# Kernel optimization log

Measured on AMD Instinct MI355X. Metric: run time of the kernel, lower is better.

Reference implementation:

```python
import jax, jax.numpy as jnp
from jax import lax
import numpy as np

B, T_IN, NF, H, T_OUT = 2048, 336, 16, 128, 168


def _gru_cell(x, h, Wih, Whh, bih, bhh):
    # PyTorch GRU cell, gate order [r, z, n]
    gi = x @ Wih.T + bih          # (B, 3H)
    gh = h @ Whh.T + bhh          # (B, 3H)
    i_r, i_z, i_n = jnp.split(gi, 3, axis=-1)
    h_r, h_z, h_n = jnp.split(gh, 3, axis=-1)
    r = jax.nn.sigmoid(i_r + h_r)
    z = jax.nn.sigmoid(i_z + h_z)
    n = jnp.tanh(i_n + r * h_n)
    return (1.0 - z) * n + z * h


def _run_gru_layer(seq_tbf, Wih, Whh, bih, bhh):
    # seq_tbf: (T, B, in_dim) -> (outputs (T,B,H), final hidden (B,H))
    h0 = jnp.zeros((seq_tbf.shape[1], H), seq_tbf.dtype)
    def step(h, xt):
        h2 = _gru_cell(xt, h, Wih, Whh, bih, bhh)
        return h2, h2
    hT, ys = lax.scan(step, h0, seq_tbf)
    return ys, hT


def setup_inputs() -> dict:
    key = jax.random.key(0)
    ks = iter(jax.random.split(key, 32))
    def w(shape, fan):
        return (jax.random.normal(next(ks), shape, jnp.float32) / np.sqrt(fan).astype(np.float32))
    inp = {"x": jax.random.normal(next(ks), (B, T_IN, NF), jnp.float32)}
    inp.update(
        enc_Wih0=w((3 * H, NF), NF), enc_Whh0=w((3 * H, H), H),
        enc_bih0=w((3 * H,), H), enc_bhh0=w((3 * H,), H),
        enc_Wih1=w((3 * H, H), H), enc_Whh1=w((3 * H, H), H),
        enc_bih1=w((3 * H,), H), enc_bhh1=w((3 * H,), H),
        dec_Wih0=w((3 * H, 1), 1), dec_Whh0=w((3 * H, H), H),
        dec_bih0=w((3 * H,), H), dec_bhh0=w((3 * H,), H),
        dec_Wih1=w((3 * H, H), H), dec_Whh1=w((3 * H, H), H),
        dec_bih1=w((3 * H,), H), dec_bhh1=w((3 * H,), H),
        fc_W1=w((H // 2, H), H), fc_b1=w((H // 2,), H),
        fc_W2=w((1, H // 2), H // 2), fc_b2=w((1,), H // 2),
    )
    return inp


def reference(x, enc_Wih0, enc_Whh0, enc_bih0, enc_bhh0,
              enc_Wih1, enc_Whh1, enc_bih1, enc_bhh1,
              dec_Wih0, dec_Whh0, dec_bih0, dec_bhh0,
              dec_Wih1, dec_Whh1, dec_bih1, dec_bhh1,
              fc_W1, fc_b1, fc_W2, fc_b2):
    b = x.shape[0]
    # --- encoder: 2-layer GRU over input sequence (eval mode: dropout off) ---
    seq = jnp.transpose(x, (1, 0, 2))                       # (T_IN, B, NF)
    ys0, h0f = _run_gru_layer(seq, enc_Wih0, enc_Whh0, enc_bih0, enc_bhh0)
    _, h1f = _run_gru_layer(ys0, enc_Wih1, enc_Whh1, enc_bih1, enc_bhh1)

    def dec_step(carry, _):
        h0, h1, inp = carry                                  # inp: (B, 1)
        h0n = _gru_cell(inp, h0, dec_Wih0, dec_Whh0, dec_bih0, dec_bhh0)
        h1n = _gru_cell(h0n, h1, dec_Wih1, dec_Whh1, dec_bih1, dec_bhh1)
        hid = jax.nn.relu(h1n @ fc_W1.T + fc_b1)
        pred = jax.nn.relu(hid @ fc_W2.T + fc_b2)            # (B, 1)
        return (h0n, h1n, pred), pred[:, 0]

    init = (h0f, h1f, jnp.zeros((b, 1), x.dtype))
    _, outs = lax.scan(dec_step, init, None, length=T_OUT)   # (T_OUT, B)
    return outs.T                                            # (B, T_OUT)
```

## Files before the change

kernel.cpp:

```cpp
#include <hip/hip_runtime.h>


typedef unsigned short ushort_t;
typedef unsigned int uint_t;
typedef __attribute__((ext_vector_type(8))) short short8;
typedef __attribute__((ext_vector_type(4))) float f32x4;

#define BT   16
#define NT   512
#define HD   128
#define TIN  336
#define TOUT 168
#define NFE  16
#define NB   128

#define SC_RZ (-1.44269504089f)
#define SC_N  (-2.88539008177f)

#define OFF_EWHH0 0
#define OFF_EWIH1 6144
#define OFF_EWHH1 12288
#define OFF_DWHH0 18432
#define OFF_DWIH1 24576
#define OFF_DWHH1 30720
#define OFF_EWIH0 36864
#define OFF_FW1   38400

__device__ __forceinline__ ushort_t f2bf(float f) {
    union { float f; uint_t u; } v; v.f = f;
    uint_t r = v.u + 0x7FFFu + ((v.u >> 16) & 1u);
    return (ushort_t)(r >> 16);
}
__device__ __forceinline__ ushort_t f2bf_h(float f) {
    union { float f; uint_t u; } v; v.f = f;
    return (ushort_t)((v.u + 0x8000u) >> 16);
}
__device__ __forceinline__ f32x4 splat4(float v) {
    return (f32x4){v, v, v, v};
}
__device__ __forceinline__ float sig2(float t) {
    return __builtin_amdgcn_rcpf(1.f + __builtin_amdgcn_exp2f(t));
}
__device__ __forceinline__ void barrier_lds() {
    asm volatile("s_waitcnt lgkmcnt(0)\n\ts_barrier" ::: "memory");
}

extern "C" __global__ __launch_bounds__(64)
void prep_kernel(const float* __restrict__ eWhh0, const float* __restrict__ eWih1,
                 const float* __restrict__ eWhh1, const float* __restrict__ dWhh0,
                 const float* __restrict__ dWih1, const float* __restrict__ dWhh1,
                 const float* __restrict__ eWih0, const float* __restrict__ fW1,
                 uint4* __restrict__ ws)
{
    const int g = blockIdx.x;
    const int L = threadIdx.x;
    const int n_lo = L & 15, q = L >> 4;

    const float* src; int n, kb, Ksrc, dst16; float sc;
    if (g < 576) {
        const int m = g / 96, lf = g % 96;
        const float* hs[6] = {eWhh0, eWih1, eWhh1, dWhh0, dWih1, dWhh1};
        src = hs[m];
        const int nt = lf >> 2, kf = lf & 3;
        n = nt * 16 + n_lo; kb = kf * 32 + q * 8; Ksrc = 128;
        dst16 = m * 6144 + lf * 64 + L;
        sc = (n < 2 * HD) ? SC_RZ : SC_N;
    } else if (g < 600) {
        const int nt = g - 576;
        src = eWih0; n = nt * 16 + n_lo; kb = q * 8; Ksrc = 16;
        dst16 = OFF_EWIH0 + nt * 64 + L;
        sc = (n < 2 * HD) ? SC_RZ : SC_N;
    } else {
        const int lf = g - 600;
        src = fW1; n = (lf >> 2) * 16 + n_lo; kb = (lf & 3) * 32 + q * 8; Ksrc = 128;
        dst16 = OFF_FW1 + lf * 64 + L;
        sc = 1.f;
    }

    ushort_t h[8];
    #pragma unroll
    for (int j = 0; j < 8; ++j) {
        const int k = kb + j;
        h[j] = (k < Ksrc) ? f2bf(sc * src[n * Ksrc + k]) : (ushort_t)0;
    }
    uint4 o;
    o.x = (uint_t)h[0] | ((uint_t)h[1] << 16);
    o.y = (uint_t)h[2] | ((uint_t)h[3] << 16);
    o.z = (uint_t)h[4] | ((uint_t)h[5] << 16);
    o.w = (uint_t)h[6] | ((uint_t)h[7] << 16);
    ws[dst16] = o;
}

__device__ __forceinline__ void combineM(const f32x4& gr, const f32x4& gz,
                                         const f32x4& gn_i, const f32x4& gn_h,
                                         float* hreg, ushort_t* wb)
{
    #pragma unroll
    for (int r_ = 0; r_ < 4; ++r_) {
        const float rg = sig2(gr[r_]);
        const float zg = sig2(gz[r_]);
        const float ng = fmaf(2.f, sig2(gn_i[r_] + rg * gn_h[r_]), -1.f);
        const float hn = fmaf(zg, hreg[r_] - ng, ng);
        hreg[r_] = hn;
        wb[r_ * 8] = f2bf_h(hn);
    }
}

extern "C" __global__ __launch_bounds__(NT, 2)
void gru_seq2seq_kernel(
    const float* __restrict__ x,
    const float* __restrict__ ebih0, const float* __restrict__ ebhh0,
    const float* __restrict__ ebih1, const float* __restrict__ ebhh1,
    const float* __restrict__ dWih0, const float* __restrict__ dbih0,
    const float* __restrict__ dbhh0,
    const float* __restrict__ dbih1, const float* __restrict__ dbhh1,
    const float* __restrict__ fb1, const float* __restrict__ fW2,
    const float* __restrict__ fb2,
    const short8* __restrict__ wf,
    float* __restrict__ out)
{
    __shared__ ushort_t h0f[2][4][512];
    __shared__ ushort_t h1f[2][4][512];
    __shared__ ushort_t xf[2][512];
    __shared__ uint4 fw1l[1024];

    const int t = threadIdx.x;
    const int L = t & 63, w = t >> 6;
    const int col16 = L & 15, q = L >> 4;
    const int col = w * 16 + col16;
    const int b0 = blockIdx.x * BT;

    for (int i = t; i < 4096; i += NT) {
        (&h0f[0][0][0])[i] = 0;
        (&h1f[0][0][0])[i] = 0;
    }
    for (int i = t; i < 1024; i += NT) (&xf[0][0])[i] = 0;

    const int kfc = col >> 5, qq = (col >> 3) & 3, jc = col & 7;
    const int hwo = kfc * 512 + (qq * 16 + q * 4) * 8 + jc;

    const int xr = t >> 4, xfeat = t & 15;
    const int xscat = (((xfeat >> 3) * 16) + (xr & 15)) * 8 + (xfeat & 7);
    float xv = (t < 256) ? x[((b0 + xr) * TIN + 0) * NFE + xfeat] : 0.f;

    const float e0_rz = SC_RZ * (ebih0[col] + ebhh0[col]);
    const float e0_zz = SC_RZ * (ebih0[HD + col] + ebhh0[HD + col]);
    const float e0_in = SC_N * ebih0[2 * HD + col];
    const float e0_hn = SC_N * ebhh0[2 * HD + col];
    const float e1_rz = SC_RZ * (ebih1[col] + ebhh1[col]);
    const float e1_zz = SC_RZ * (ebih1[HD + col] + ebhh1[HD + col]);
    const float e1_in = SC_N * ebih1[2 * HD + col];
    const float e1_hn = SC_N * ebhh1[2 * HD + col];

    float h0r[4] = {0, 0, 0, 0};
    float h1r[4] = {0, 0, 0, 0};

    short8 Wa[3][4], Wb[3][4], Wc[3][4];
    short8 We[3];
    #pragma unroll
    for (int t3 = 0; t3 < 3; ++t3) {
        const int nt = w + t3 * 8;
        We[t3] = wf[OFF_EWIH0 + nt * 64 + L];
        #pragma unroll
        for (int kf = 0; kf < 4; ++kf) {
            Wa[t3][kf] = wf[OFF_EWHH0 + (nt * 4 + kf) * 64 + L];
            Wb[t3][kf] = wf[OFF_EWIH1 + (nt * 4 + kf) * 64 + L];
            Wc[t3][kf] = wf[OFF_EWHH1 + (nt * 4 + kf) * 64 + L];
        }
    }

    barrier_lds();
    if (t < 256) {
        (&xf[0][0])[xscat] = f2bf_h(xv);
        xv = x[((b0 + xr) * TIN + 1) * NFE + xfeat];
    }
    barrier_lds();

    {
        if (t < 256) {
            (&xf[0][0])[512 + xscat] = f2bf_h(xv);
            xv = x[((b0 + xr) * TIN + 2) * NFE + xfeat];
        }
        const short8 Ax = *(const short8*)&xf[0][L * 8];
        short8 Ah[4];
        #pragma unroll
        for (int kf = 0; kf < 4; ++kf)
            Ah[kf] = *(const short8*)&h0f[0][kf][L * 8];
        f32x4 gr = splat4(e0_rz), gz = splat4(e0_zz);
        f32x4 gni = splat4(e0_in), gnh = splat4(e0_hn);
        #pragma unroll
        for (int kf = 0; kf < 4; ++kf) {
            gr  = __builtin_amdgcn_mfma_f32_16x16x32_bf16(Ah[kf], Wa[0][kf], gr,  0, 0, 0);
            gz  = __builtin_amdgcn_mfma_f32_16x16x32_bf16(Ah[kf], Wa[1][kf], gz,  0, 0, 0);
            gnh = __builtin_amdgcn_mfma_f32_16x16x32_bf16(Ah[kf], Wa[2][kf], gnh, 0, 0, 0);
        }
        gr  = __builtin_amdgcn_mfma_f32_16x16x32_bf16(Ax, We[0], gr,  0, 0, 0);
        gz  = __builtin_amdgcn_mfma_f32_16x16x32_bf16(Ax, We[1], gz,  0, 0, 0);
        gni = __builtin_amdgcn_mfma_f32_16x16x32_bf16(Ax, We[2], gni, 0, 0, 0);
        combineM(gr, gz, gni, gnh, h0r, &(&h0f[0][0][0])[2048 + hwo]);
        barrier_lds();
    }

    for (int i = 1; i < TIN; ++i) {
        const int p = i & 1;
        if (t < 256 && i + 1 < TIN) {
            (&xf[0][0])[(1 - p) * 512 + xscat] = f2bf_h(xv);
            if (i + 2 < TIN) xv = x[((b0 + xr) * TIN + i + 2) * NFE + xfeat];
        }
        const short8 Ax = *(const short8*)&xf[p][L * 8];
        short8 Ah0[4], Ah1[4];
        #pragma unroll
        for (int kf = 0; kf < 4; ++kf) {
            Ah0[kf] = *(const short8*)&h0f[p][kf][L * 8];
            Ah1[kf] = *(const short8*)&h1f[p][kf][L * 8];
        }
        f32x4 a_r = splat4(e0_rz), a_z = splat4(e0_zz);
        f32x4 a_ni = splat4(e0_in), a_nh = splat4(e0_hn);
        f32x4 b_r = splat4(e1_rz), b_z = splat4(e1_zz);
        f32x4 b_ni = splat4(e1_in), b_nh = splat4(e1_hn);
        #pragma unroll
        for (int kf = 0; kf < 4; ++kf) {
            a_r  = __builtin_amdgcn_mfma_f32_16x16x32_bf16(Ah0[kf], Wa[0][kf], a_r,  0, 0, 0);
            a_z  = __builtin_amdgcn_mfma_f32_16x16x32_bf16(Ah0[kf], Wa[1][kf], a_z,  0, 0, 0);
            a_nh = __builtin_amdgcn_mfma_f32_16x16x32_bf16(Ah0[kf], Wa[2][kf], a_nh, 0, 0, 0);
            b_r  = __builtin_amdgcn_mfma_f32_16x16x32_bf16(Ah0[kf], Wb[0][kf], b_r,  0, 0, 0);
            b_z  = __builtin_amdgcn_mfma_f32_16x16x32_bf16(Ah0[kf], Wb[1][kf], b_z,  0, 0, 0);
            b_ni = __builtin_amdgcn_mfma_f32_16x16x32_bf16(Ah0[kf], Wb[2][kf], b_ni, 0, 0, 0);
            b_r  = __builtin_amdgcn_mfma_f32_16x16x32_bf16(Ah1[kf], Wc[0][kf], b_r,  0, 0, 0);
            b_z  = __builtin_amdgcn_mfma_f32_16x16x32_bf16(Ah1[kf], Wc[1][kf], b_z,  0, 0, 0);
            b_nh = __builtin_amdgcn_mfma_f32_16x16x32_bf16(Ah1[kf], Wc[2][kf], b_nh, 0, 0, 0);
        }
        a_r  = __builtin_amdgcn_mfma_f32_16x16x32_bf16(Ax, We[0], a_r,  0, 0, 0);
        a_z  = __builtin_amdgcn_mfma_f32_16x16x32_bf16(Ax, We[1], a_z,  0, 0, 0);
        a_ni = __builtin_amdgcn_mfma_f32_16x16x32_bf16(Ax, We[2], a_ni, 0, 0, 0);

        combineM(a_r, a_z, a_ni, a_nh, h0r, &(&h0f[0][0][0])[(1 - p) * 2048 + hwo]);
        combineM(b_r, b_z, b_ni, b_nh, h1r, &(&h1f[0][0][0])[(1 - p) * 2048 + hwo]);
        barrier_lds();
    }

    {
        short8 Ai[4], Ah[4];
        #pragma unroll
        for (int kf = 0; kf < 4; ++kf) {
            Ai[kf] = *(const short8*)&h0f[0][kf][L * 8];
            Ah[kf] = *(const short8*)&h1f[0][kf][L * 8];
        }
        f32x4 gr = splat4(e1_rz), gz = splat4(e1_zz);
        f32x4 gni = splat4(e1_in), gnh = splat4(e1_hn);
        #pragma unroll
        for (int kf = 0; kf < 4; ++kf) {
            gr  = __builtin_amdgcn_mfma_f32_16x16x32_bf16(Ai[kf], Wb[0][kf], gr,  0, 0, 0);
            gz  = __builtin_amdgcn_mfma_f32_16x16x32_bf16(Ai[kf], Wb[1][kf], gz,  0, 0, 0);
            gni = __builtin_amdgcn_mfma_f32_16x16x32_bf16(Ai[kf], Wb[2][kf], gni, 0, 0, 0);
            gr  = __builtin_amdgcn_mfma_f32_16x16x32_bf16(Ah[kf], Wc[0][kf], gr,  0, 0, 0);
            gz  = __builtin_amdgcn_mfma_f32_16x16x32_bf16(Ah[kf], Wc[1][kf], gz,  0, 0, 0);
            gnh = __builtin_amdgcn_mfma_f32_16x16x32_bf16(Ah[kf], Wc[2][kf], gnh, 0, 0, 0);
        }
        combineM(gr, gz, gni, gnh, h1r, &(&h1f[0][0][0])[2048 + hwo]);
        barrier_lds();
    }

    asm volatile("" ::: "memory");

    #pragma unroll
    for (int t3 = 0; t3 < 3; ++t3) {
        const int nt = w + t3 * 8;
        #pragma unroll
        for (int kf = 0; kf < 4; ++kf) {
            Wa[t3][kf] = wf[OFF_DWHH0 + (nt * 4 + kf) * 64 + L];
            Wb[t3][kf] = wf[OFF_DWIH1 + (nt * 4 + kf) * 64 + L];
            Wc[t3][kf] = wf[OFF_DWHH1 + (nt * 4 + kf) * 64 + L];
        }
    }
    for (int i = t; i < 1024; i += NT) fw1l[i] = ((const uint4*)wf)[OFF_FW1 + i];

    const float d0_rz = SC_RZ * (dbih0[col] + dbhh0[col]);
    const float d0_zz = SC_RZ * (dbih0[HD + col] + dbhh0[HD + col]);
    const float d0_in = SC_N * dbih0[2 * HD + col];
    const float d0_hn = SC_N * dbhh0[2 * HD + col];
    const float d1_rz = SC_RZ * (dbih1[col] + dbhh1[col]);
    const float d1_zz = SC_RZ * (dbih1[HD + col] + dbhh1[HD + col]);
    const float d1_in = SC_N * dbih1[2 * HD + col];
    const float d1_hn = SC_N * dbhh1[2 * HD + col];
    const float w0r = SC_RZ * dWih0[col];
    const float w0z = SC_RZ * dWih0[HD + col];
    const float w0n = SC_N * dWih0[2 * HD + col];
    float f1bv[4], w2v[4];
    #pragma unroll
    for (int nt = 0; nt < 4; ++nt) {
        f1bv[nt] = fb1[nt * 16 + col16];
        w2v[nt]  = fW2[nt * 16 + col16];
    }
    const float fb2v = fb2[0];
    float ivr[4] = {0.f, 0.f, 0.f, 0.f};

    {
        short8 Ah[4];
        #pragma unroll
        for (int kf = 0; kf < 4; ++kf)
            Ah[kf] = *(const short8*)&h0f[0][kf][L * 8];
        f32x4 g0 = splat4(d0_rz), g1 = splat4(d0_zz), g2 = splat4(d0_hn);
        #pragma unroll
        for (int kf = 0; kf < 4; ++kf) {
            g0 = __builtin_amdgcn_mfma_f32_16x16x32_bf16(Ah[kf], Wa[0][kf], g0, 0, 0, 0);
            g1 = __builtin_amdgcn_mfma_f32_16x16x32_bf16(Ah[kf], Wa[1][kf], g1, 0, 0, 0);
            g2 = __builtin_amdgcn_mfma_f32_16x16x32_bf16(Ah[kf], Wa[2][kf], g2, 0, 0, 0);
        }
        barrier_lds();
        ushort_t* wb = &(&h0f[0][0][0])[0 + hwo];
        #pragma unroll
        for (int r_ = 0; r_ < 4; ++r_) {
            const float rg = sig2(g0[r_]);
            const float zg = sig2(g1[r_]);
            const float ng = fmaf(2.f, sig2(d0_in + rg * g2[r_]), -1.f);
            const float hn = fmaf(zg, h0r[r_] - ng, ng);
            h0r[r_] = hn;
            wb[r_ * 8] = f2bf_h(hn);
        }
    }
    barrier_lds();

    for (int s = 0; s < TOUT; ++s) {
        const int p = s & 1;

        {
            short8 Ai[4], Ah[4];
            #pragma unroll
            for (int kf = 0; kf < 4; ++kf) {
                Ai[kf] = *(const short8*)&h0f[p][kf][L * 8];
                Ah[kf] = *(const short8*)&h1f[1 - p][kf][L * 8];
            }
            f32x4 gr = splat4(d1_rz), gz = splat4(d1_zz);
            f32x4 gni = splat4(d1_in), gnh = splat4(d1_hn);
            #pragma unroll
            for (int kf = 0; kf < 4; ++kf) {
                gr  = __builtin_amdgcn_mfma_f32_16x16x32_bf16(Ai[kf], Wb[0][kf], gr,  0, 0, 0);
                gz  = __builtin_amdgcn_mfma_f32_16x16x32_bf16(Ai[kf], Wb[1][kf], gz,  0, 0, 0);
                gni = __builtin_amdgcn_mfma_f32_16x16x32_bf16(Ai[kf], Wb[2][kf], gni, 0, 0, 0);
                gr  = __builtin_amdgcn_mfma_f32_16x16x32_bf16(Ah[kf], Wc[0][kf], gr,  0, 0, 0);
                gz  = __builtin_amdgcn_mfma_f32_16x16x32_bf16(Ah[kf], Wc[1][kf], gz,  0, 0, 0);
                gnh = __builtin_amdgcn_mfma_f32_16x16x32_bf16(Ah[kf], Wc[2][kf], gnh, 0, 0, 0);
            }
            combineM(gr, gz, gni, gnh, h1r, &(&h1f[0][0][0])[p * 2048 + hwo]);
        }
        barrier_lds();

        {
            short8 Af[4], Ah[4];
            #pragma unroll
            for (int kf = 0; kf < 4; ++kf) {
                Af[kf] = *(const short8*)&h1f[p][kf][L * 8];
                Ah[kf] = *(const short8*)&h0f[p][kf][L * 8];
            }
            f32x4 g0 = splat4(d0_rz), g1 = splat4(d0_zz), g2 = splat4(d0_hn);
            f32x4 fc[4];
            #pragma unroll
            for (int nt = 0; nt < 4; ++nt) fc[nt] = splat4(0.f);
            #pragma unroll
            for (int kf = 0; kf < 4; ++kf) {
                g0 = __builtin_amdgcn_mfma_f32_16x16x32_bf16(Ah[kf], Wa[0][kf], g0, 0, 0, 0);
                g1 = __builtin_amdgcn_mfma_f32_16x16x32_bf16(Ah[kf], Wa[1][kf], g1, 0, 0, 0);
                g2 = __builtin_amdgcn_mfma_f32_16x16x32_bf16(Ah[kf], Wa[2][kf], g2, 0, 0, 0);
                #pragma unroll
                for (int nt = 0; nt < 4; ++nt) {
                    const short8 b = *(const short8*)&fw1l[(nt * 4 + kf) * 64 + L];
                    fc[nt] = __builtin_amdgcn_mfma_f32_16x16x32_bf16(Af[kf], b, fc[nt], 0, 0, 0);
                }
            }
            float ps[4];
            #pragma unroll
            for (int r_ = 0; r_ < 4; ++r_) {
                float s_ = 0.f;
                #pragma unroll
                for (int nt = 0; nt < 4; ++nt)
                    s_ = fmaf(fmaxf(fc[nt][r_] + f1bv[nt], 0.f), w2v[nt], s_);
                ps[r_] = s_;
            }
            #pragma unroll
            for (int r_ = 0; r_ < 4; ++r_) {
                ps[r_] += __shfl_xor(ps[r_], 1, 64);
                ps[r_] += __shfl_xor(ps[r_], 2, 64);
                ps[r_] += __shfl_xor(ps[r_], 4, 64);
                ps[r_] += __shfl_xor(ps[r_], 8, 64);
                ivr[r_] = fmaxf(ps[r_] + fb2v, 0.f);
            }
            if (w == 0 && col16 == 0) {
                #pragma unroll
                for (int r_ = 0; r_ < 4; ++r_)
                    out[(b0 + q * 4 + r_) * TOUT + s] = ivr[r_];
            }
            ushort_t* wb = &(&h0f[0][0][0])[(1 - p) * 2048 + hwo];
            #pragma unroll
            for (int r_ = 0; r_ < 4; ++r_) {
                const float iv = ivr[r_];
                const float rg = sig2(fmaf(iv, w0r, g0[r_]));
                const float zg = sig2(fmaf(iv, w0z, g1[r_]));
                const float tt = fmaf(iv, w0n, d0_in) + rg * g2[r_];
                const float ng = fmaf(2.f, sig2(tt), -1.f);
                const float hn = fmaf(zg, h0r[r_] - ng, ng);
                h0r[r_] = hn;
                wb[r_ * 8] = f2bf_h(hn);
            }
        }
        barrier_lds();
    }
}

extern "C" void kernel_launch(void* const* d_in, const int* in_sizes, int n_in,
                              void* d_out, int out_size, void* d_ws, size_t ws_size,
                              hipStream_t stream) {
    const float* x     = (const float*)d_in[0];
    const float* eWih0 = (const float*)d_in[1];
    const float* eWhh0 = (const float*)d_in[2];
    const float* ebih0 = (const float*)d_in[3];
    const float* ebhh0 = (const float*)d_in[4];
    const float* eWih1 = (const float*)d_in[5];
    const float* eWhh1 = (const float*)d_in[6];
    const float* ebih1 = (const float*)d_in[7];
    const float* ebhh1 = (const float*)d_in[8];
    const float* dWih0 = (const float*)d_in[9];
    const float* dWhh0 = (const float*)d_in[10];
    const float* dbih0 = (const float*)d_in[11];
    const float* dbhh0 = (const float*)d_in[12];
    const float* dWih1 = (const float*)d_in[13];
    const float* dWhh1 = (const float*)d_in[14];
    const float* dbih1 = (const float*)d_in[15];
    const float* dbhh1 = (const float*)d_in[16];
    const float* fW1   = (const float*)d_in[17];
    const float* fb1   = (const float*)d_in[18];
    const float* fW2   = (const float*)d_in[19];
    const float* fb2   = (const float*)d_in[20];
    float* out = (float*)d_out;

    hipLaunchKernelGGL(prep_kernel, dim3(616), dim3(64), 0, stream,
                       eWhh0, eWih1, eWhh1, dWhh0, dWih1, dWhh1, eWih0, fW1,
                       (uint4*)d_ws);
    hipLaunchKernelGGL(gru_seq2seq_kernel, dim3(NB), dim3(NT), 0, stream,
                       x, ebih0, ebhh0, ebih1, ebhh1,
                       dWih0, dbih0, dbhh0, dbih1, dbhh1,
                       fb1, fW2, fb2,
                       (const short8*)d_ws, out);
}
```

Before: 819.7 us.

## Halve batch tile to 8 rows and redistribute MFMA outputs via permlane32 swap

Reduces the per-block batch tile from 16 to 8 rows so twice as many blocks are launched (256 instead of 128), spreading the sequential recurrence across more CUs. Because the 16x16 MFMA tile now holds only 8 valid rows, permlane32_swap moves accumulator elements between the lane halves so each lane handles two gate elements instead of four, halving the transcendental work per lane. The price is that half of each MFMA's rows are wasted and extra cross-lane swaps are added on the critical path of every timestep.

```diff
diff --git a/kernel.cpp b/kernel.cpp
--- a/kernel.cpp
+++ b/kernel.cpp
@@ -5,14 +5,15 @@
 typedef unsigned int uint_t;
 typedef __attribute__((ext_vector_type(8))) short short8;
 typedef __attribute__((ext_vector_type(4))) float f32x4;
-
-#define BT   16
+typedef __attribute__((ext_vector_type(2))) unsigned int uintx2;
+
+#define BT   8
 #define NT   512
 #define HD   128
 #define TIN  336
 #define TOUT 168
 #define NFE  16
-#define NB   128
+#define NB   256
 
 #define SC_RZ (-1.44269504089f)
 #define SC_N  (-2.88539008177f)
@@ -43,6 +44,20 @@
 }
 __device__ __forceinline__ void barrier_lds() {
     asm volatile("s_waitcnt lgkmcnt(0)\n\ts_barrier" ::: "memory");
+}
+
+__device__ __forceinline__ void pl32swap(float& a, float& b) {
+    uintx2 r = __builtin_amdgcn_permlane32_swap(
+        __float_as_uint(a), __float_as_uint(b), false, false);
+    a = __uint_as_float(r[0]);
+    b = __uint_as_float(r[1]);
+}
+__device__ __forceinline__ void spread2(f32x4 v, float& e0, float& e1) {
+    float a0 = v[0], a2 = v[2];
+    float a1 = v[1], a3 = v[3];
+    pl32swap(a0, a2);
+    pl32swap(a1, a3);
+    e0 = a0; e1 = a1;
 }
 
 extern "C" __global__ __launch_bounds__(64)
@@ -91,18 +106,23 @@
     ws[dst16] = o;
 }
 
-__device__ __forceinline__ void combineM(const f32x4& gr, const f32x4& gz,
+__device__ __forceinline__ void combineS(const f32x4& gr, const f32x4& gz,
                                          const f32x4& gn_i, const f32x4& gn_h,
                                          float* hreg, ushort_t* wb)
 {
+    float r_[2], z_[2], i_[2], n_[2];
+    spread2(gr,   r_[0], r_[1]);
+    spread2(gz,   z_[0], z_[1]);
+    spread2(gn_i, i_[0], i_[1]);
+    spread2(gn_h, n_[0], n_[1]);
     #pragma unroll
-    for (int r_ = 0; r_ < 4; ++r_) {
-        const float rg = sig2(gr[r_]);
-        const float zg = sig2(gz[r_]);
-        const float ng = fmaf(2.f, sig2(gn_i[r_] + rg * gn_h[r_]), -1.f);
-        const float hn = fmaf(zg, hreg[r_] - ng, ng);
-        hreg[r_] = hn;
-        wb[r_ * 8] = f2bf_h(hn);
+    for (int e = 0; e < 2; ++e) {
+        const float rg = sig2(r_[e]);
+        const float zg = sig2(z_[e]);
+        const float ng = fmaf(2.f, sig2(i_[e] + rg * n_[e]), -1.f);
+        const float hn = fmaf(zg, hreg[e] - ng, ng);
+        hreg[e] = hn;
+        wb[e * 8] = f2bf_h(hn);
     }
 }
 
@@ -137,11 +157,12 @@
     for (int i = t; i < 1024; i += NT) (&xf[0][0])[i] = 0;
 
     const int kfc = col >> 5, qq = (col >> 3) & 3, jc = col & 7;
-    const int hwo = kfc * 512 + (qq * 16 + q * 4) * 8 + jc;
+    const int hi2 = (L >> 5) * 2;
+    const int hwoE = kfc * 512 + (qq * 16 + (q & 1) * 4 + hi2) * 8 + jc;
 
     const int xr = t >> 4, xfeat = t & 15;
     const int xscat = (((xfeat >> 3) * 16) + (xr & 15)) * 8 + (xfeat & 7);
-    float xv = (t < 256) ? x[((b0 + xr) * TIN + 0) * NFE + xfeat] : 0.f;
+    float xv = (t < 128) ? x[((b0 + xr) * TIN + 0) * NFE + xfeat] : 0.f;
 
     const float e0_rz = SC_RZ * (ebih0[col] + ebhh0[col]);
     const float e0_zz = SC_RZ * (ebih0[HD + col] + ebhh0[HD + col]);
@@ -152,8 +173,8 @@
     const float e1_in = SC_N * ebih1[2 * HD + col];
     const float e1_hn = SC_N * ebhh1[2 * HD + col];
 
-    float h0r[4] = {0, 0, 0, 0};
-    float h1r[4] = {0, 0, 0, 0};
+    float h0r[2] = {0, 0};
+    float h1r[2] = {0, 0};
 
     short8 Wa[3][4], Wb[3][4], Wc[3][4];
     short8 We[3];
@@ -170,14 +191,14 @@
     }
 
     barrier_lds();
-    if (t < 256) {
+    if (t < 128) {
         (&xf[0][0])[xscat] = f2bf_h(xv);
         xv = x[((b0 + xr) * TIN + 1) * NFE + xfeat];
     }
     barrier_lds();
 
     {
-        if (t < 256) {
+        if (t < 128) {
             (&xf[0][0])[512 + xscat] = f2bf_h(xv);
             xv = x[((b0 + xr) * TIN + 2) * NFE + xfeat];
         }
@@ -197,13 +218,13 @@
         gr  = __builtin_amdgcn_mfma_f32_16x16x32_bf16(Ax, We[0], gr,  0, 0, 0);
         gz  = __builtin_amdgcn_mfma_f32_16x16x32_bf16(Ax, We[1], gz,  0, 0, 0);
         gni = __builtin_amdgcn_mfma_f32_16x16x32_bf16(Ax, We[2], gni, 0, 0, 0);
-        combineM(gr, gz, gni, gnh, h0r, &(&h0f[0][0][0])[2048 + hwo]);
+        combineS(gr, gz, gni, gnh, h0r, &(&h0f[0][0][0])[2048 + hwoE]);
         barrier_lds();
     }
 
     for (int i = 1; i < TIN; ++i) {
         const int p = i & 1;
-        if (t < 256 && i + 1 < TIN) {
+        if (t < 128 && i + 1 < TIN) {
             (&xf[0][0])[(1 - p) * 512 + xscat] = f2bf_h(xv);
             if (i + 2 < TIN) xv = x[((b0 + xr) * TIN + i + 2) * NFE + xfeat];
         }
@@ -234,8 +255,8 @@
         a_z  = __builtin_amdgcn_mfma_f32_16x16x32_bf16(Ax, We[1], a_z,  0, 0, 0);
         a_ni = __builtin_amdgcn_mfma_f32_16x16x32_bf16(Ax, We[2], a_ni, 0, 0, 0);
 
-        combineM(a_r, a_z, a_ni, a_nh, h0r, &(&h0f[0][0][0])[(1 - p) * 2048 + hwo]);
-        combineM(b_r, b_z, b_ni, b_nh, h1r, &(&h1f[0][0][0])[(1 - p) * 2048 + hwo]);
+        combineS(a_r, a_z, a_ni, a_nh, h0r, &(&h0f[0][0][0])[(1 - p) * 2048 + hwoE]);
+        combineS(b_r, b_z, b_ni, b_nh, h1r, &(&h1f[0][0][0])[(1 - p) * 2048 + hwoE]);
         barrier_lds();
     }
 
@@ -257,7 +278,7 @@
             gz  = __builtin_amdgcn_mfma_f32_16x16x32_bf16(Ah[kf], Wc[1][kf], gz,  0, 0, 0);
             gnh = __builtin_amdgcn_mfma_f32_16x16x32_bf16(Ah[kf], Wc[2][kf], gnh, 0, 0, 0);
         }
-        combineM(gr, gz, gni, gnh, h1r, &(&h1f[0][0][0])[2048 + hwo]);
+        combineS(gr, gz, gni, gnh, h1r, &(&h1f[0][0][0])[2048 + hwoE]);
         barrier_lds();
     }
 
@@ -293,7 +314,7 @@
         w2v[nt]  = fW2[nt * 16 + col16];
     }
     const float fb2v = fb2[0];
-    float ivr[4] = {0.f, 0.f, 0.f, 0.f};
+    float ivr[2] = {0.f, 0.f};
 
     {
         short8 Ah[4];
@@ -307,16 +328,20 @@
             g1 = __builtin_amdgcn_mfma_f32_16x16x32_bf16(Ah[kf], Wa[1][kf], g1, 0, 0, 0);
             g2 = __builtin_amdgcn_mfma_f32_16x16x32_bf16(Ah[kf], Wa[2][kf], g2, 0, 0, 0);
         }
-        barrier_lds();
-        ushort_t* wb = &(&h0f[0][0][0])[0 + hwo];
-        #pragma unroll
-        for (int r_ = 0; r_ < 4; ++r_) {
-            const float rg = sig2(g0[r_]);
-            const float zg = sig2(g1[r_]);
-            const float ng = fmaf(2.f, sig2(d0_in + rg * g2[r_]), -1.f);
-            const float hn = fmaf(zg, h0r[r_] - ng, ng);
-            h0r[r_] = hn;
-            wb[r_ * 8] = f2bf_h(hn);
+        float g0e[2], g1e[2], g2e[2];
+        spread2(g0, g0e[0], g0e[1]);
+        spread2(g1, g1e[0], g1e[1]);
+        spread2(g2, g2e[0], g2e[1]);
+        barrier_lds();
+        ushort_t* wb = &(&h0f[0][0][0])[0 + hwoE];
+        #pragma unroll
+        for (int e = 0; e < 2; ++e) {
+            const float rg = sig2(g0e[e]);
+            const float zg = sig2(g1e[e]);
+            const float ng = fmaf(2.f, sig2(d0_in + rg * g2e[e]), -1.f);
+            const float hn = fmaf(zg, h0r[e] - ng, ng);
+            h0r[e] = hn;
+            wb[e * 8] = f2bf_h(hn);
         }
     }
     barrier_lds();
@@ -342,7 +367,7 @@
                 gz  = __builtin_amdgcn_mfma_f32_16x16x32_bf16(Ah[kf], Wc[1][kf], gz,  0, 0, 0);
                 gnh = __builtin_amdgcn_mfma_f32_16x16x32_bf16(Ah[kf], Wc[2][kf], gnh, 0, 0, 0);
             }
-            combineM(gr, gz, gni, gnh, h1r, &(&h1f[0][0][0])[p * 2048 + hwo]);
+            combineS(gr, gz, gni, gnh, h1r, &(&h1f[0][0][0])[p * 2048 + hwoE]);
         }
         barrier_lds();
 
@@ -368,39 +393,47 @@
                     fc[nt] = __builtin_amdgcn_mfma_f32_16x16x32_bf16(Af[kf], b, fc[nt], 0, 0, 0);
                 }
             }
-            float ps[4];
-            #pragma unroll
-            for (int r_ = 0; r_ < 4; ++r_) {
+            float g0e[2], g1e[2], g2e[2], fe0[4], fe1[4];
+            spread2(g0, g0e[0], g0e[1]);
+            spread2(g1, g1e[0], g1e[1]);
+            spread2(g2, g2e[0], g2e[1]);
+            #pragma unroll
+            for (int nt = 0; nt < 4; ++nt) spread2(fc[nt], fe0[nt], fe1[nt]);
+            float ps[2];
+            #pragma unroll
+            for (int e = 0; e < 2; ++e) {
                 float s_ = 0.f;
                 #pragma unroll
-                for (int nt = 0; nt < 4; ++nt)
-                    s_ = fmaf(fmaxf(fc[nt][r_] + f1bv[nt], 0.f), w2v[nt], s_);
-                ps[r_] = s_;
-            }
-            #pragma unroll
-            for (int r_ = 0; r_ < 4; ++r_) {
-                ps[r_] += __shfl_xor(ps[r_], 1, 64);
-                ps[r_] += __shfl_xor(ps[r_], 2, 64);
-                ps[r_] += __shfl_xor(ps[r_], 4, 64);
-                ps[r_] += __shfl_xor(ps[r_], 8, 64);
-                ivr[r_] = fmaxf(ps[r_] + fb2v, 0.f);
+                for (int nt = 0; nt < 4; ++nt) {
+                    const float v = (e == 0) ? fe0[nt] : fe1[nt];
+                    s_ = fmaf(fmaxf(v + f1bv[nt], 0.f), w2v[nt], s_);
+                }
+                ps[e] = s_;
+            }
+            #pragma unroll
+            for (int e = 0; e < 2; ++e) {
+                ps[e] += __shfl_xor(ps[e], 1, 64);
+                ps[e] += __shfl_xor(ps[e], 2, 64);
+                ps[e] += __shfl_xor(ps[e], 4, 64);
+                ps[e] += __shfl_xor(ps[e], 8, 64);
+                ivr[e] = fmaxf(ps[e] + fb2v, 0.f);
             }
             if (w == 0 && col16 == 0) {
                 #pragma unroll
-                for (int r_ = 0; r_ < 4; ++r_)
-                    out[(b0 + q * 4 + r_) * TOUT + s] = ivr[r_];
-            }
-            ushort_t* wb = &(&h0f[0][0][0])[(1 - p) * 2048 + hwo];
-            #pragma unroll
-            for (int r_ = 0; r_ < 4; ++r_) {
-                const float iv = ivr[r_];
-                const float rg = sig2(fmaf(iv, w0r, g0[r_]));
-                const float zg = sig2(fmaf(iv, w0z, g1[r_]));
-                const float tt = fmaf(iv, w0n, d0_in) + rg * g2[r_];
+                for (int e = 0; e < 2; ++e)
+                    out[(b0 + (q & 1) * 4 + hi2 + e) * TOUT + s] = ivr[e];
+            }
+            ushort_t* wb = &(&h0f[0][0][0])[(1 - p) * 2048 + hwoE];
+            #pragma unroll
+            for (int e = 0; e < 2; ++e) {
+                const float iv = ivr[e];
+                const float rg = sig2(fmaf(iv, w0r, g0e[e]));
+                const float zg = sig2(fmaf(iv, w0z, g1e[e]));
+                const float tt = fmaf(iv, w0n, d0_in) + rg * g2e[e];
                 const float ng = fmaf(2.f, sig2(tt), -1.f);
-                const float hn = fmaf(zg, h0r[r_] - ng, ng);
-                h0r[r_] = hn;
-                wb[r_ * 8] = f2bf_h(hn);
+                const float hn = fmaf(zg, h0r[e] - ng, ng);
+                h0r[e] = hn;
+                wb[e * 8] = f2bf_h(hn);
             }
         }
         barrier_lds();
```

Result: faster. 740.9 us (-9.6%).
